# Kernel optimization log

Hardware: AMD Instinct MI355X
Metric: run time of the kernel (lower is better)

Reference implementation:

```python
import math
import jax, jax.numpy as jnp
import numpy as np

C = 256
CQ = C // 8
B, H, W = 8, 64, 64


def setup_inputs() -> dict:
    key = jax.random.key(0)
    k1, k2, k3, k4 = jax.random.split(key, 4)
    x = jax.random.normal(k1, (B, C, H, W), dtype=jnp.float32)
    # 1x1 conv weights, bias=False -> plain [out, in] matrices
    wq = jax.random.normal(k2, (CQ, C), dtype=jnp.float32) * 0.02
    wk = jax.random.normal(k3, (CQ, C), dtype=jnp.float32) * 0.02
    wv = jax.random.normal(k4, (C, C), dtype=jnp.float32) * 0.02
    # gamma init is zeros in the torch module; use small nonzero so output depends on attention path
    gamma = jnp.ones((1,), dtype=jnp.float32) * 0.5
    return {"x": x, "wq": wq, "wk": wk, "wv": wv, "gamma": gamma}


def reference(x, wq, wk, wv, gamma):
    b, c, h, w = x.shape
    n = h * w
    xr = x.reshape(b, c, n)                       # [B, C, N]
    q = jnp.einsum('oc,bcn->bon', wq, xr)         # [B, Cq, N]
    k = jnp.einsum('oc,bcn->bon', wk, xr)         # [B, Cq, N]
    v = jnp.einsum('oc,bcn->bon', wv, xr)         # [B, C, N]
    # attn[b, i, j] = softmax_j( q[:, i] . k[:, j] / sqrt(Cq) )
    scores = jnp.einsum('bci,bcj->bij', q, k) / math.sqrt(q.shape[1])  # [B, N, N]
    attn = jax.nn.softmax(scores, axis=-1)
    # out[b, c, m] = sum_n v[b, c, n] * attn[b, m, n]
    out = jnp.einsum('bcn,bmn->bcm', v, attn).reshape(b, c, h, w)
    return gamma[0] * out + x
```

## Files before the change

kernel.cpp:

```cpp
#include <hip/hip_runtime.h>

#define B_ 8
#define C_ 256
#define CQ_ 32
#define N_ 4096

typedef __attribute__((ext_vector_type(8))) short short8;
typedef __attribute__((ext_vector_type(4))) float float4v;

#define QSCALE 0.2550599232f

#if __has_builtin(__builtin_amdgcn_exp2f)
#define EXP2F __builtin_amdgcn_exp2f
#else
#define EXP2F exp2f
#endif

static __device__ __forceinline__ unsigned short f2bf(float f) {
  unsigned int u = __float_as_uint(f);
  u += 0x7FFFu + ((u >> 16) & 1u);
  return (unsigned short)(u >> 16);
}

static __device__ __forceinline__ void async16(void* lds, const void* g) {
  __builtin_amdgcn_global_load_lds(
      (const __attribute__((address_space(1))) unsigned int*)g,
      (__attribute__((address_space(3))) unsigned int*)lds, 16, 0, 0);
}

__global__ __launch_bounds__(256) void wconv_kernel(
    const float* __restrict__ wq, const float* __restrict__ wk,
    const float* __restrict__ wv, unsigned short* __restrict__ w_bf) {
  int o = blockIdx.x * 8 + (threadIdx.x >> 5);
  int c8 = (threadIdx.x & 31) * 8;
  const float* src; float sc = 1.f;
  if (o < 32)      { src = wq + (size_t)o * 256; sc = QSCALE; }
  else if (o < 64) { src = wk + (size_t)(o - 32) * 256; }
  else             { src = wv + (size_t)(o - 64) * 256; }
  float4 a = *(const float4*)(src + c8);
  float4 bq = *(const float4*)(src + c8 + 4);
  unsigned short t[8] = {f2bf(a.x*sc), f2bf(a.y*sc), f2bf(a.z*sc), f2bf(a.w*sc),
                         f2bf(bq.x*sc), f2bf(bq.y*sc), f2bf(bq.z*sc), f2bf(bq.w*sc)};
  *(uint4*)(w_bf + (size_t)o * 256 + c8) = *(const uint4*)t;
}

__global__ __launch_bounds__(256, 2) void proj_kernel(
    const float* __restrict__ x, const unsigned short* __restrict__ w_bf,
    unsigned short* __restrict__ qT, unsigned short* __restrict__ kT,
    unsigned short* __restrict__ v) {
  __shared__ __align__(16) unsigned short xb[2][64 * 32];
  int tid = threadIdx.x, wave = tid >> 6, lane = tid & 63;
  int q16 = lane >> 4, l16 = lane & 15;
  int b = blockIdx.x, n0 = blockIdx.y * 64;

  int p = tid & 15, n4g = tid >> 4;
  const float* x0 = x + (size_t)b * C_ * N_ + n0 + n4g * 4;

  auto stage = [&](int buf, int ks) {
    const float* r0 = x0 + (size_t)(ks * 32 + 2 * p) * N_;
    float4 fa = *(const float4*)(r0);
    float4 fb = *(const float4*)(r0 + N_);
    float va[4] = {fa.x, fa.y, fa.z, fa.w};
    float vb[4] = {fb.x, fb.y, fb.z, fb.w};
    #pragma unroll
    for (int i = 0; i < 4; ++i) {
      int n = n4g * 4 + i;
      unsigned int pk = (unsigned int)f2bf(va[i]) | ((unsigned int)f2bf(vb[i]) << 16);
      int so = (p >> 2) ^ ((n >> 1) & 3);
      *(unsigned int*)(&xb[buf][n * 32 + so * 8 + (p & 3) * 2]) = pk;
    }
  };

  float4v acc[5][4];
  float4v zerov = {0.f, 0.f, 0.f, 0.f};
  #pragma unroll
  for (int mt = 0; mt < 5; ++mt)
    for (int nt = 0; nt < 4; ++nt) acc[mt][nt] = zerov;

  stage(0, 0);
  __syncthreads();

  int o0 = wave * 80;
  int sxo = (q16 ^ ((l16 >> 1) & 3)) * 8;
  #pragma unroll 1
  for (int ks = 0; ks < 8; ++ks) {
    if (ks < 7) stage((ks + 1) & 1, ks + 1);
    short8 af[5], bf4[4];
    #pragma unroll
    for (int mt = 0; mt < 5; ++mt)
      af[mt] = *(const short8*)(w_bf + (size_t)(o0 + mt * 16 + l16) * 256 + ks * 32 + q16 * 8);
    #pragma unroll
    for (int nt = 0; nt < 4; ++nt)
      bf4[nt] = *(const short8*)(&xb[ks & 1][(nt * 16 + l16) * 32 + sxo]);
    #pragma unroll
    for (int mt = 0; mt < 5; ++mt)
      #pragma unroll
      for (int nt = 0; nt < 4; ++nt)
        acc[mt][nt] = __builtin_amdgcn_mfma_f32_16x16x32_bf16(af[mt], bf4[nt], acc[mt][nt], 0, 0, 0);
    __syncthreads();
  }

  #pragma unroll
  for (int mt = 0; mt < 5; ++mt) {
    int og = o0 + mt * 16 + q16 * 4;
    #pragma unroll
    for (int nt = 0; nt < 4; ++nt) {
      int n = n0 + nt * 16 + l16;
      unsigned short t[4];
      if (og < 64) {
        #pragma unroll
        for (int r = 0; r < 4; ++r) t[r] = f2bf(acc[mt][nt][r]);
        unsigned short* dst = (og < 32) ? (qT + ((size_t)b * N_ + n) * CQ_ + og)
                                        : (kT + ((size_t)b * N_ + n) * CQ_ + (og - 32));
        *(uint2*)dst = *(const uint2*)t;
      } else {
        #pragma unroll
        for (int r = 0; r < 4; ++r)
          v[((size_t)b * C_ + og - 64 + r) * N_ + n] = f2bf(acc[mt][nt][r]);
      }
    }
  }
}

__global__ __launch_bounds__(512, 2) void attn_kernel(
    const unsigned short* __restrict__ qT, const unsigned short* __restrict__ kT,
    const unsigned short* __restrict__ v, const float* __restrict__ x,
    const float* __restrict__ gamma, float* __restrict__ out) {
  __shared__ __align__(16) unsigned short v_lds[256 * 64];
  __shared__ __align__(16) unsigned short kt_lds[2][64 * 32];
  __shared__ __align__(16) unsigned short p_lds[128 * 64];
  __shared__ float l_lds[128];

  int tid = threadIdx.x, wave = tid >> 6, lane = tid & 63;
  int q16 = lane >> 4, l16 = lane & 15;
  int bid = blockIdx.x, b = bid & 7, m0 = (bid >> 3) * 128;

  short8 qfrag = *(const short8*)(qT + ((size_t)b * N_ + m0 + wave * 16 + l16) * CQ_ + q16 * 8);

  const unsigned short* vbase = v + (size_t)b * C_ * N_;
  auto stageV = [&](int j0) {
    #pragma unroll
    for (int it = 0; it < 4; ++it) {
      int r = wave * 32 + it * 8 + (lane >> 3);
      int lo = (lane & 7) ^ (lane >> 3);
      async16(&v_lds[(wave * 32 + it * 8) * 64], vbase + (size_t)r * N_ + j0 + lo * 8);
    }
  };
  auto stageK = [&](int buf, int j0) {
    if (wave >= 4) {
      int w4 = wave - 4;
      int r = w4 * 16 + (lane >> 2);
      int lo = (lane & 3) ^ ((r >> 1) & 3);
      async16(&kt_lds[buf][w4 * 16 * 32], kT + ((size_t)b * N_ + j0 + r) * CQ_ + lo * 8);
    }
  };

  stageK(0, 0);
  stageV(0);
  __syncthreads();

  float4v acc[4][4];
  float4v zerov = {0.f, 0.f, 0.f, 0.f};
  #pragma unroll
  for (int mt = 0; mt < 4; ++mt)
    for (int ct = 0; ct < 4; ++ct) acc[mt][ct] = zerov;
  float lrun[4] = {0.f, 0.f, 0.f, 0.f};

  int kro = q16 ^ ((l16 >> 1) & 3);
  int vro = l16 & 7;
  int lo8 = l16 >> 3, li = l16 & 7;
  int h = wave >> 2, cq = wave & 3;

  for (int j = 0; j < 64; ++j) {
    int cur = j & 1;
    float4v s[4];
    #pragma unroll
    for (int jt = 0; jt < 4; ++jt) {
      short8 kf = *(const short8*)(&kt_lds[cur][(jt * 16 + l16) * 32 + kro * 8]);
      s[jt] = __builtin_amdgcn_mfma_f32_16x16x32_bf16(qfrag, kf, zerov, 0, 0, 0);
    }

    #pragma unroll
    for (int r = 0; r < 4; ++r) {
      float p0 = EXP2F(s[0][r]), p1 = EXP2F(s[1][r]);
      float p2 = EXP2F(s[2][r]), p3 = EXP2F(s[3][r]);
      lrun[r] += (p0 + p1) + (p2 + p3);
      int prow = wave * 16 + q16 * 4 + r;
      int rl = (q16 * 4 + r) & 7;
      unsigned short* pr = &p_lds[prow * 64 + li];
      int o0 = lo8 ^ rl;
      pr[(o0 ^ 0) * 8] = (unsigned short)(__float_as_uint(p0) >> 16);
      pr[(o0 ^ 2) * 8] = (unsigned short)(__float_as_uint(p1) >> 16);
      pr[(o0 ^ 4) * 8] = (unsigned short)(__float_as_uint(p2) >> 16);
      pr[(o0 ^ 6) * 8] = (unsigned short)(__float_as_uint(p3) >> 16);
    }
    if (j == 63) {
      #pragma unroll
      for (int r = 0; r < 4; ++r) {
        float t = lrun[r];
        t += __shfl_xor(t, 1); t += __shfl_xor(t, 2);
        t += __shfl_xor(t, 4); t += __shfl_xor(t, 8);
        if (l16 == 0) l_lds[wave * 16 + q16 * 4 + r] = t;
      }
    }
    __syncthreads();

    if (j < 63) stageK(cur ^ 1, (j + 1) * 64);

    #pragma unroll
    for (int ks = 0; ks < 2; ++ks) {
      short8 pf[4], vf[4];
      #pragma unroll
      for (int mt = 0; mt < 4; ++mt)
        pf[mt] = *(const short8*)(&p_lds[(h * 64 + mt * 16 + l16) * 64 + ((ks * 4 + q16) ^ vro) * 8]);
      #pragma unroll
      for (int ct = 0; ct < 4; ++ct)
        vf[ct] = *(const short8*)(&v_lds[(cq * 64 + ct * 16 + l16) * 64 + ((ks * 4 + q16) ^ vro) * 8]);
      #pragma unroll
      for (int mt = 0; mt < 4; ++mt)
        #pragma unroll
        for (int ct = 0; ct < 4; ++ct)
          acc[mt][ct] = __builtin_amdgcn_mfma_f32_16x16x32_bf16(pf[mt], vf[ct], acc[mt][ct], 0, 0, 0);
    }
    __syncthreads();

    if (j < 63) stageV((j + 1) * 64);
  }

  float g = gamma[0];
  #pragma unroll
  for (int mt = 0; mt < 4; ++mt) {
    float linv[4];
    #pragma unroll
    for (int r = 0; r < 4; ++r) linv[r] = 1.f / l_lds[h * 64 + mt * 16 + q16 * 4 + r];
    int n = m0 + h * 64 + mt * 16 + q16 * 4;
    #pragma unroll
    for (int ct = 0; ct < 4; ++ct) {
      int c = cq * 64 + ct * 16 + l16;
      size_t off = ((size_t)b * C_ + c) * N_ + n;
      float4 xv = *(const float4*)(x + off);
      float4 o;
      o.x = g * acc[mt][ct][0] * linv[0] + xv.x;
      o.y = g * acc[mt][ct][1] * linv[1] + xv.y;
      o.z = g * acc[mt][ct][2] * linv[2] + xv.z;
      o.w = g * acc[mt][ct][3] * linv[3] + xv.w;
      *(float4*)(out + off) = o;
    }
  }
}

extern "C" void kernel_launch(void* const* d_in, const int* in_sizes, int n_in,
                              void* d_out, int out_size, void* d_ws, size_t ws_size,
                              hipStream_t stream) {
  const float* x     = (const float*)d_in[0];
  const float* wq    = (const float*)d_in[1];
  const float* wk    = (const float*)d_in[2];
  const float* wv    = (const float*)d_in[3];
  const float* gamma = (const float*)d_in[4];
  float* out = (float*)d_out;

  unsigned short* qT  = (unsigned short*)d_ws;
  unsigned short* kT  = qT + (size_t)B_ * N_ * CQ_;
  unsigned short* vv  = kT + (size_t)B_ * N_ * CQ_;
  unsigned short* wbf = vv + (size_t)B_ * C_ * N_;

  hipLaunchKernelGGL(wconv_kernel, dim3(40), dim3(256), 0, stream, wq, wk, wv, wbf);
  hipLaunchKernelGGL(proj_kernel, dim3(8, 64), dim3(256), 0, stream, x, wbf, qT, kT, vv);
  hipLaunchKernelGGL(attn_kernel, dim3(256), dim3(512), 0, stream, qT, kT, vv, x, gamma, out);
}
```

Measured before the change: 192.1 us.

## Double-buffer V and P in attention, drop a barrier, retile projection kernel

The attention kernel now double-buffers the V and P shared-memory tiles and prefetches K two steps ahead, which removes the second barrier per iteration so staging overlaps the PV MFMAs. The residual x is loaded into registers a few iterations before the end. The projection kernel processes 128 pixels per block with output channels split across the grid, and restages x via lane shuffles into wider LDS stores. The larger LDS footprint and extra held registers may reduce occupancy of the attention kernel.

```diff
diff --git a/kernel.cpp b/kernel.cpp
--- a/kernel.cpp
+++ b/kernel.cpp
@@ -48,26 +48,45 @@
     const float* __restrict__ x, const unsigned short* __restrict__ w_bf,
     unsigned short* __restrict__ qT, unsigned short* __restrict__ kT,
     unsigned short* __restrict__ v) {
-  __shared__ __align__(16) unsigned short xb[2][64 * 32];
+  __shared__ __align__(16) unsigned short xb[2][128 * 32];
   int tid = threadIdx.x, wave = tid >> 6, lane = tid & 63;
   int q16 = lane >> 4, l16 = lane & 15;
-  int b = blockIdx.x, n0 = blockIdx.y * 64;
-
-  int p = tid & 15, n4g = tid >> 4;
-  const float* x0 = x + (size_t)b * C_ * N_ + n0 + n4g * 4;
+  int b = blockIdx.x, n0 = blockIdx.y * 128, oh = blockIdx.z;
+  int op = wave >> 1, nh = wave & 1;
+  int o0 = oh * 160 + op * 80;
+
+  int p = lane >> 5, m = lane & 31;
+  const float* xrow = x + (size_t)b * C_ * N_ + n0 + 4 * m;
 
   auto stage = [&](int buf, int ks) {
-    const float* r0 = x0 + (size_t)(ks * 32 + 2 * p) * N_;
-    float4 fa = *(const float4*)(r0);
-    float4 fb = *(const float4*)(r0 + N_);
-    float va[4] = {fa.x, fa.y, fa.z, fa.w};
-    float vb[4] = {fb.x, fb.y, fb.z, fb.w};
-    #pragma unroll
-    for (int i = 0; i < 4; ++i) {
-      int n = n4g * 4 + i;
-      unsigned int pk = (unsigned int)f2bf(va[i]) | ((unsigned int)f2bf(vb[i]) << 16);
-      int so = (p >> 2) ^ ((n >> 1) & 3);
-      *(unsigned int*)(&xb[buf][n * 32 + so * 8 + (p & 3) * 2]) = pk;
+    #pragma unroll
+    for (int tp = 0; tp < 2; ++tp) {
+      int c0 = wave * 8 + tp * 4;
+      const float* basep = xrow + (size_t)(ks * 32 + c0 + p) * N_;
+      float4 f0 = *(const float4*)(basep);
+      float4 f1 = *(const float4*)(basep + 2 * N_);
+      unsigned int a0 = (unsigned int)f2bf(f0.x) | ((unsigned int)f2bf(f1.x) << 16);
+      unsigned int a1 = (unsigned int)f2bf(f0.y) | ((unsigned int)f2bf(f1.y) << 16);
+      unsigned int a2 = (unsigned int)f2bf(f0.z) | ((unsigned int)f2bf(f1.z) << 16);
+      unsigned int a3 = (unsigned int)f2bf(f0.w) | ((unsigned int)f2bf(f1.w) << 16);
+      unsigned int X = p ? a0 : a2;
+      unsigned int Y = p ? a1 : a3;
+      X = __shfl_xor(X, 32);
+      Y = __shfl_xor(Y, 32);
+      #pragma unroll
+      for (int e = 0; e < 2; ++e) {
+        unsigned int mi = p ? (e ? a3 : a2) : (e ? a1 : a0);
+        unsigned int th = e ? Y : X;
+        unsigned int lo = p ? th : mi;
+        unsigned int hi = p ? mi : th;
+        unsigned int w0 = (lo & 0xffffu) | (hi << 16);
+        unsigned int w1 = (lo >> 16) | (hi & 0xffff0000u);
+        int jj = 2 * p + e;
+        int n = 4 * m + jj;
+        int oct = (c0 >> 3) ^ jj ^ (m & 3);
+        unsigned int off = n * 32 + oct * 8 + (c0 & 7);
+        *(uint2*)(&xb[buf][off]) = make_uint2(w0, w1);
+      }
     }
   };
 
@@ -80,8 +99,7 @@
   stage(0, 0);
   __syncthreads();
 
-  int o0 = wave * 80;
-  int sxo = (q16 ^ ((l16 >> 1) & 3)) * 8;
+  int fx = (l16 & 3) ^ (l16 >> 2);
   #pragma unroll 1
   for (int ks = 0; ks < 8; ++ks) {
     if (ks < 7) stage((ks + 1) & 1, ks + 1);
@@ -91,7 +109,7 @@
       af[mt] = *(const short8*)(w_bf + (size_t)(o0 + mt * 16 + l16) * 256 + ks * 32 + q16 * 8);
     #pragma unroll
     for (int nt = 0; nt < 4; ++nt)
-      bf4[nt] = *(const short8*)(&xb[ks & 1][(nt * 16 + l16) * 32 + sxo]);
+      bf4[nt] = *(const short8*)(&xb[ks & 1][(nh * 64 + nt * 16 + l16) * 32 + ((q16 ^ fx) * 8)]);
     #pragma unroll
     for (int mt = 0; mt < 5; ++mt)
       #pragma unroll
@@ -105,7 +123,7 @@
     int og = o0 + mt * 16 + q16 * 4;
     #pragma unroll
     for (int nt = 0; nt < 4; ++nt) {
-      int n = n0 + nt * 16 + l16;
+      int n = n0 + nh * 64 + nt * 16 + l16;
       unsigned short t[4];
       if (og < 64) {
         #pragma unroll
@@ -126,9 +144,9 @@
     const unsigned short* __restrict__ qT, const unsigned short* __restrict__ kT,
     const unsigned short* __restrict__ v, const float* __restrict__ x,
     const float* __restrict__ gamma, float* __restrict__ out) {
-  __shared__ __align__(16) unsigned short v_lds[256 * 64];
+  __shared__ __align__(16) unsigned short v_lds[2][256 * 64];
   __shared__ __align__(16) unsigned short kt_lds[2][64 * 32];
-  __shared__ __align__(16) unsigned short p_lds[128 * 64];
+  __shared__ __align__(16) unsigned short p_lds[2][128 * 64];
   __shared__ float l_lds[128];
 
   int tid = threadIdx.x, wave = tid >> 6, lane = tid & 63;
@@ -138,12 +156,12 @@
   short8 qfrag = *(const short8*)(qT + ((size_t)b * N_ + m0 + wave * 16 + l16) * CQ_ + q16 * 8);
 
   const unsigned short* vbase = v + (size_t)b * C_ * N_;
-  auto stageV = [&](int j0) {
+  auto stageV = [&](int buf, int j0) {
     #pragma unroll
     for (int it = 0; it < 4; ++it) {
       int r = wave * 32 + it * 8 + (lane >> 3);
       int lo = (lane & 7) ^ (lane >> 3);
-      async16(&v_lds[(wave * 32 + it * 8) * 64], vbase + (size_t)r * N_ + j0 + lo * 8);
+      async16(&v_lds[buf][(wave * 32 + it * 8) * 64], vbase + (size_t)r * N_ + j0 + lo * 8);
     }
   };
   auto stageK = [&](int buf, int j0) {
@@ -156,7 +174,8 @@
   };
 
   stageK(0, 0);
-  stageV(0);
+  stageK(1, 64);
+  stageV(0, 0);
   __syncthreads();
 
   float4v acc[4][4];
@@ -165,12 +184,14 @@
   for (int mt = 0; mt < 4; ++mt)
     for (int ct = 0; ct < 4; ++ct) acc[mt][ct] = zerov;
   float lrun[4] = {0.f, 0.f, 0.f, 0.f};
+  float4 xpre[4][4];
 
   int kro = q16 ^ ((l16 >> 1) & 3);
   int vro = l16 & 7;
   int lo8 = l16 >> 3, li = l16 & 7;
   int h = wave >> 2, cq = wave & 3;
 
+  #pragma unroll 2
   for (int j = 0; j < 64; ++j) {
     int cur = j & 1;
     float4v s[4];
@@ -187,7 +208,7 @@
       lrun[r] += (p0 + p1) + (p2 + p3);
       int prow = wave * 16 + q16 * 4 + r;
       int rl = (q16 * 4 + r) & 7;
-      unsigned short* pr = &p_lds[prow * 64 + li];
+      unsigned short* pr = &p_lds[cur][prow * 64 + li];
       int o0 = lo8 ^ rl;
       pr[(o0 ^ 0) * 8] = (unsigned short)(__float_as_uint(p0) >> 16);
       pr[(o0 ^ 2) * 8] = (unsigned short)(__float_as_uint(p1) >> 16);
@@ -205,26 +226,34 @@
     }
     __syncthreads();
 
-    if (j < 63) stageK(cur ^ 1, (j + 1) * 64);
+    if (j < 63) stageV(cur ^ 1, (j + 1) * 64);
+    if (j < 62) stageK(cur, (j + 2) * 64);
+    if (j == 60) {
+      #pragma unroll
+      for (int mt = 0; mt < 4; ++mt)
+        #pragma unroll
+        for (int ct = 0; ct < 4; ++ct) {
+          int n = m0 + h * 64 + mt * 16 + q16 * 4;
+          int c = cq * 64 + ct * 16 + l16;
+          xpre[mt][ct] = *(const float4*)(x + ((size_t)b * C_ + c) * N_ + n);
+        }
+    }
 
     #pragma unroll
     for (int ks = 0; ks < 2; ++ks) {
       short8 pf[4], vf[4];
       #pragma unroll
       for (int mt = 0; mt < 4; ++mt)
-        pf[mt] = *(const short8*)(&p_lds[(h * 64 + mt * 16 + l16) * 64 + ((ks * 4 + q16) ^ vro) * 8]);
+        pf[mt] = *(const short8*)(&p_lds[cur][(h * 64 + mt * 16 + l16) * 64 + ((ks * 4 + q16) ^ vro) * 8]);
       #pragma unroll
       for (int ct = 0; ct < 4; ++ct)
-        vf[ct] = *(const short8*)(&v_lds[(cq * 64 + ct * 16 + l16) * 64 + ((ks * 4 + q16) ^ vro) * 8]);
+        vf[ct] = *(const short8*)(&v_lds[cur][(cq * 64 + ct * 16 + l16) * 64 + ((ks * 4 + q16) ^ vro) * 8]);
       #pragma unroll
       for (int mt = 0; mt < 4; ++mt)
         #pragma unroll
         for (int ct = 0; ct < 4; ++ct)
           acc[mt][ct] = __builtin_amdgcn_mfma_f32_16x16x32_bf16(pf[mt], vf[ct], acc[mt][ct], 0, 0, 0);
     }
-    __syncthreads();
-
-    if (j < 63) stageV((j + 1) * 64);
   }
 
   float g = gamma[0];
@@ -238,7 +267,7 @@
     for (int ct = 0; ct < 4; ++ct) {
       int c = cq * 64 + ct * 16 + l16;
       size_t off = ((size_t)b * C_ + c) * N_ + n;
-      float4 xv = *(const float4*)(x + off);
+      float4 xv = xpre[mt][ct];
       float4 o;
       o.x = g * acc[mt][ct][0] * linv[0] + xv.x;
       o.y = g * acc[mt][ct][1] * linv[1] + xv.y;
@@ -265,6 +294,6 @@
   unsigned short* wbf = vv + (size_t)B_ * C_ * N_;
 
   hipLaunchKernelGGL(wconv_kernel, dim3(40), dim3(256), 0, stream, wq, wk, wv, wbf);
-  hipLaunchKernelGGL(proj_kernel, dim3(8, 64), dim3(256), 0, stream, x, wbf, qT, kT, vv);
+  hipLaunchKernelGGL(proj_kernel, dim3(8, 32, 2), dim3(256), 0, stream, x, wbf, qT, kT, vv);
   hipLaunchKernelGGL(attn_kernel, dim3(256), dim3(512), 0, stream, qT, kT, vv, x, gamma, out);
 }
```

New measurement: 200.7 us. 1.04x slower.
